# Kernel optimization log

Measured on AMD Instinct MI355X. Metric: run time of the kernel, lower is better.

Reference implementation:

```python
import jax, jax.numpy as jnp
import numpy as np

NEG = -1e20  # finite stand-in for -inf (exp underflows to 0; avoids nan grads)
S_RANGE = 19   # prune_range hard-coded in the module
TERM = 0       # termination/blank symbol
LM_ONLY = 0.25 # lm_only_scale; am_only_scale = 0 so that branch vanishes


def _mi(px, py):
    """RNN-T mutual-information forward DP (fast_rnnt mutual_information_recursion).
    px: (B,S,T+1) logprob of emitting symbol s+1 at (s,t); py: (B,S+1,T) blank logprobs.
    p[b,s,t] = logaddexp(p[b,s-1,t]+px[b,s-1,t], p[b,s,t-1]+py[b,s,t-1]); returns p[:,S,T]."""
    B, S, T1 = px.shape
    p0 = jnp.concatenate([jnp.zeros((B, 1), px.dtype),
                          jnp.cumsum(py[:, 0, :], axis=1)], axis=1)  # row s=0: (B,T+1)
    def outer(p_prev, inp):
        px_s, py_s = inp                 # (B,T+1), (B,T)
        b = p_prev + px_s                # vertical (emit) path into next row
        def inner(c, xs):
            b_t, py_t = xs
            c = jnp.logaddexp(b_t, c + py_t)
            return c, c
        _, rest = jax.lax.scan(inner, b[:, 0], (b[:, 1:].T, py_s.T))  # rest: (T,B)
        p_row = jnp.concatenate([b[:, :1], rest.T], axis=1)
        return p_row, None
    p_last, _ = jax.lax.scan(outer, p0,
                             (jnp.moveaxis(px, 1, 0), jnp.moveaxis(py[:, 1:, :], 1, 0)))
    return p_last[:, -1]  # (B,) total log-prob at (S,T)


def _smoothed_logprobs(am, lm, symbols):
    """fast_rnnt.get_rnnt_logprobs_smoothed with lm_only_scale=0.25, am_only_scale=0."""
    B, T, C = am.shape
    S = symbols.shape[1]
    lm_max = jnp.max(lm, axis=2, keepdims=True)   # (B,S+1,1)
    am_max = jnp.max(am, axis=2, keepdims=True)   # (B,T,1)
    lm_p = jnp.exp(lm - lm_max)
    am_p = jnp.exp(am - am_max)
    # normalizers[b,s,t] = log sum_k exp(lm[b,s,k] + am[b,t,k]) via matmul trick
    normalizers = jnp.log(jnp.einsum('bsc,btc->bst', lm_p, am_p)) \
        + lm_max + jnp.swapaxes(am_max, 1, 2)     # (B,S+1,T)
    sym_b = jnp.broadcast_to(symbols[:, None, :], (B, T, S))
    px_am = jnp.swapaxes(jnp.take_along_axis(am, sym_b, axis=2), 1, 2)  # (B,S,T)
    px_lm = jnp.take_along_axis(lm[:, :S], symbols[:, :, None], axis=2)  # (B,S,1)
    px = px_am + px_lm - normalizers[:, :S, :]
    lm_lsm = jax.nn.log_softmax(lm, axis=2)
    px_lmonly = jnp.take_along_axis(lm_lsm[:, :S], symbols[:, :, None], axis=2)
    comb = 1.0 - LM_ONLY
    px_i = comb * px + LM_ONLY * px_lmonly
    px_i = jnp.concatenate([px_i, jnp.full((B, S, 1), NEG, px_i.dtype)], axis=2)  # (B,S,T+1)
    py = am[:, :, TERM][:, None, :] + lm[:, :, TERM][:, :, None] - normalizers
    py_i = comb * py + LM_ONLY * lm_lsm[:, :, TERM][:, :, None]  # (B,S+1,T)
    return px_i, py_i


def _suffix_min(x):  # fast_rnnt _monotonic_lower_bound: x[t] = min(x[t:])
    return jax.lax.associative_scan(jnp.minimum, x, axis=1, reverse=True)


def _adjust_lower_bound(s_begin, r):  # fast_rnnt _adjust_pruning_lower_bound
    Tn = s_begin.shape[1]
    s_begin = _suffix_min(s_begin)
    off = (r - 1) * jnp.arange(Tn, dtype=s_begin.dtype)
    y = -(s_begin - off)
    y = jnp.maximum(_suffix_min(y), 0)
    return -(y - off)


def _prune_ranges(px_grad, py_grad, r):
    """fast_rnnt.get_rnnt_prune_ranges (all sequences full length)."""
    B, S, T1 = px_grad.shape
    T = T1 - 1
    py_pad = jnp.concatenate([py_grad, jnp.zeros((B, S + 1, 1), py_grad.dtype)], axis=2)
    tot = jnp.concatenate([px_grad, jnp.zeros((B, 1, T1), px_grad.dtype)], axis=1) + py_pad
    tot = jnp.concatenate([jnp.zeros((B, 1, T1), tot.dtype), tot], axis=1)  # (B,S+2,T1)
    cs = jnp.cumsum(tot, axis=1)
    diff = cs[:, r:, :] - cs[:, :-r, :]  # windowed occupancy sums
    s_begin = jnp.argmax(diff, axis=1)[:, :T].astype(jnp.int32)
    s_begin = _adjust_lower_bound(s_begin, r)
    return s_begin[:, :, None] + jnp.arange(r, dtype=jnp.int32)[None, None, :]  # (B,T,r)


def _pruned_logprobs(logits, symbols, ranges):
    """fast_rnnt.get_rnnt_logprobs_pruned."""
    B, T, r, C = logits.shape
    S = symbols.shape[1]
    norm = jax.nn.logsumexp(logits, axis=3)  # (B,T,r)
    sym_t = jnp.concatenate([symbols, jnp.full((B, 1), TERM, symbols.dtype)], axis=1)
    sym_b = jnp.broadcast_to(sym_t[:, None, :], (B, T, S + 1))
    pruned_sym = jnp.take_along_axis(sym_b, ranges, axis=2)  # (B,T,r)
    px = jnp.take_along_axis(logits, pruned_sym[..., None], axis=3)[..., 0] - norm
    py = logits[..., TERM] - norm
    def to_full(x):  # scatter (B,T,r) band into absolute symbol positions (B,T,S+1)
        pad = jnp.full((B, T, S + 1 - r), NEG, x.dtype)
        xf = jnp.concatenate([x, pad], axis=2)
        idx = (jnp.arange(S + 1)[None, None, :] - ranges[:, :, 0:1]) % (S + 1)
        return jnp.take_along_axis(xf, idx, axis=2)
    px_f = jnp.swapaxes(to_full(px), 1, 2)  # (B,S+1,T)
    py_f = jnp.swapaxes(to_full(py), 1, 2)  # (B,S+1,T)
    px_f = jnp.concatenate([px_f, jnp.full((B, S + 1, 1), NEG, px_f.dtype)], axis=2)[:, :S, :]
    return px_f, py_f  # (B,S,T+1), (B,S+1,T)


def _forward(am, lm, targets, joiner_w, joiner_b):
    px, py = _smoothed_logprobs(am, lm, targets)
    simple_loss = -jnp.mean(_mi(px, py))  # reduction='mean'
    # occupation-probability grads (values only, used for pruning)
    gpx, gpy = jax.grad(lambda a: jnp.sum(_mi(a[0], a[1])))(
        (jax.lax.stop_gradient(px), jax.lax.stop_gradient(py)))
    ranges = _prune_ranges(gpx, gpy, S_RANGE)  # (B,T,19) int32, constant wrt grads
    lm_pruned = jax.vmap(lambda l, rg: l[rg])(lm, ranges)  # (B,T,r,C) gather
    # joiner: logits = Linear(tanh(am_pruned + lm_pruned)); am broadcast over r
    logits = jnp.einsum('btrc,cd->btrd',
                        jnp.tanh(am[:, :, None, :] + lm_pruned), joiner_w) + joiner_b
    px2, py2 = _pruned_logprobs(logits.astype(jnp.float32), targets, ranges)
    pruned_loss = -jnp.mean(_mi(px2, py2))
    return 0.1 * simple_loss + pruned_loss


def setup_inputs() -> dict:
    key = jax.random.key(0)
    k = jax.random.split(key, 5)
    B, T, S, C = 8, 512, 128, 512
    return {
        "am": jax.random.normal(k[0], (B, T, C), jnp.float32),
        "lm": jax.random.normal(k[1], (B, S + 1, C), jnp.float32),
        "targets": jax.random.randint(k[2], (B, S), 1, C),  # blank=0 excluded
        "y_lens": jnp.full((B,), S, jnp.int32),             # full-length boundaries
        "joiner_w": 0.05 * jax.random.normal(k[3], (C, C), jnp.float32),
        "joiner_b": jnp.zeros((C,), jnp.float32),
    }


def reference(am, lm, targets, y_lens, joiner_w, joiner_b):
    # boundary = [0, 0, y_lens(=S), T] for every sequence
    return _forward(am, lm, targets, joiner_w, joiner_b)
```

## Files before the change

### kernel.cpp

```cpp
#include <hip/hip_runtime.h>
#include <math.h>

#define NEGV -1e20f
#define DPAD 132
#define RBOFF 16
#define ROWSA 676
#define RB(p,b) ((p) + ((size_t)(b) * ROWSA + RBOFF) * DPAD)

typedef __attribute__((ext_vector_type(4))) float floatx4;
typedef __attribute__((ext_vector_type(8))) short short8;
typedef __attribute__((ext_vector_type(4))) short short4v;


__device__ __forceinline__ float lae(float a, float b){
  float mx = fmaxf(a, b);
  float mn = fminf(a, b);
  return mx + __logf(1.f + __expf(mn - mx));
}

__device__ __forceinline__ short f2bf(float x){
  union { float f; unsigned u; } v; v.f = x;
  unsigned r = v.u + 0x7fffu + ((v.u >> 16) & 1u);
  return (short)(r >> 16);
}

__device__ __forceinline__ float fast_tanh(float x){
  x = fminf(fmaxf(x, -15.f), 15.f);
  float e = __expf(2.f * x);
  return (e - 1.f) / (e + 1.f);
}

__global__ __launch_bounds__(256) void k_row_stats(
    const float* __restrict__ in, float* __restrict__ outMax, float* __restrict__ outLse)
{
  int row = blockIdx.x;
  const float* r = in + (size_t)row * 512;
  int tid = threadIdx.x;
  float v0 = r[tid], v1 = r[tid + 256];
  float m = fmaxf(v0, v1);
  #pragma unroll
  for (int off = 32; off; off >>= 1) m = fmaxf(m, __shfl_xor(m, off, 64));
  __shared__ float sm[4];
  __shared__ float sbm;
  int wv = tid >> 6;
  if ((tid & 63) == 0) sm[wv] = m;
  __syncthreads();
  if (tid == 0) sbm = fmaxf(fmaxf(sm[0], sm[1]), fmaxf(sm[2], sm[3]));
  __syncthreads();
  float mx = sbm;
  if (tid == 0) outMax[row] = mx;
  if (outLse){
    float s = __expf(v0 - mx) + __expf(v1 - mx);
    #pragma unroll
    for (int off = 32; off; off >>= 1) s += __shfl_xor(s, off, 64);
    __shared__ float sp[4];
    if ((tid & 63) == 0) sp[wv] = s;
    __syncthreads();
    if (tid == 0) outLse[row] = mx + __logf(sp[0] + sp[1] + sp[2] + sp[3]);
  }
}

__global__ __launch_bounds__(256) void k_wb(const float* __restrict__ W, short* __restrict__ Wb){
  int idx = blockIdx.x * 256 + threadIdx.x;
  int d = idx >> 9, c = idx & 511;
  Wb[idx] = f2bf(W[c * 512 + d]);
}

__global__ __launch_bounds__(256) void k_norm(
    const float* __restrict__ am, const float* __restrict__ lm,
    const float* __restrict__ lmMax, const float* __restrict__ amMax,
    float* __restrict__ normv)
{
  int b = blockIdx.z;
  int s0 = blockIdx.y * 16;
  int t0 = blockIdx.x * 128;
  __shared__ float lmS[16][68];
  __shared__ float amS[128][68];
  int tid = threadIdx.x;
  int ts = tid >> 4, tt = tid & 15;
  float acc[8];
  #pragma unroll
  for (int j = 0; j < 8; ++j) acc[j] = 0.f;

  for (int k0 = 0; k0 < 512; k0 += 64){
    {
      int e = tid * 4;
      int rr = e >> 6, cc = e & 63;
      int s = s0 + rr;
      floatx4 o = {0.f, 0.f, 0.f, 0.f};
      if (s < 129){
        float mx = lmMax[b * 129 + s];
        floatx4 v = *(const floatx4*)(lm + ((size_t)(b * 129 + s)) * 512 + k0 + cc);
        o[0] = __expf(v[0] - mx); o[1] = __expf(v[1] - mx);
        o[2] = __expf(v[2] - mx); o[3] = __expf(v[3] - mx);
      }
      *(floatx4*)&lmS[rr][cc] = o;
    }
    #pragma unroll
    for (int i = 0; i < 8; ++i){
      int e = (tid + i * 256) * 4;
      int rr = e >> 6, cc = e & 63;
      float mx = amMax[b * 512 + t0 + rr];
      floatx4 v = *(const floatx4*)(am + ((size_t)(b * 512 + t0 + rr)) * 512 + k0 + cc);
      floatx4 o;
      o[0] = __expf(v[0] - mx); o[1] = __expf(v[1] - mx);
      o[2] = __expf(v[2] - mx); o[3] = __expf(v[3] - mx);
      *(floatx4*)&amS[rr][cc] = o;
    }
    __syncthreads();
    #pragma unroll 4
    for (int k = 0; k < 64; ++k){
      float a = lmS[ts][k];
      #pragma unroll
      for (int j = 0; j < 8; ++j) acc[j] += a * amS[tt + 16 * j][k];
    }
    __syncthreads();
  }
  int s = s0 + ts;
  if (s < 129){
    float lmx = lmMax[b * 129 + s];
    #pragma unroll
    for (int j = 0; j < 8; ++j){
      int t = t0 + tt + 16 * j;
      normv[((size_t)(b * 129 + s)) * 512 + t] = __logf(acc[j]) + lmx + amMax[b * 512 + t];
    }
  }
}

__global__ __launch_bounds__(256) void k_pxpy(
    const float* __restrict__ am, const float* __restrict__ lm,
    const int* __restrict__ targets, const float* __restrict__ normv,
    const float* __restrict__ lmLse, float* __restrict__ pxd, float* __restrict__ pyd)
{
  int bs = blockIdx.x;
  int b = bs / 129, s = bs % 129;
  float lm0 = lm[(size_t)bs * 512];
  float lse = lmLse[bs];
  int sym = 0; float lms = 0.f;
  if (s < 128){ sym = targets[b * 128 + s]; lms = lm[(size_t)bs * 512 + sym]; }
  const float* nrm = normv + (size_t)bs * 512;
  float* pydb = RB(pyd, b);
  float* pxdb = RB(pxd, b);
  for (int t = threadIdx.x; t < 513; t += 256){
    if (t < 512){
      float n = nrm[t];
      float a0 = am[((size_t)(b * 512 + t)) * 512];
      pydb[(size_t)(s + t) * DPAD + s] = 0.75f * (a0 + lm0 - n) + 0.25f * (lm0 - lse);
      if (s < 128){
        float as = am[((size_t)(b * 512 + t)) * 512 + sym];
        pxdb[(size_t)(s + t) * DPAD + s] = 0.75f * (as + lms - n) + 0.25f * (lms - lse);
      }
    } else if (s < 128){
      pxdb[(size_t)(s + 512) * DPAD + s] = NEGV;
    }
  }
}


__device__ __forceinline__ void dp_fwd_run(
    const float* __restrict__ pxb, const float* __restrict__ pyb,
    float* __restrict__ pab, float* __restrict__ tot, int b)
{
  int l = threadIdx.x;
  const int a = 2 * l;
  float curA = NEGV, curB = NEGV, curC = NEGV, send = NEGV;
  int paddr = (l - 1) << 2;

  float2 cpx = *(const float2*)(pxb - DPAD + a);
  float2 cpy = *(const float2*)(pyb - DPAD + a);
  float  cpz = pyb[-DPAD + 128];

  float2 b0px[8], b0py[8], b1px[8], b1py[8];
  float  b0pz[8], b1pz[8];
  float  outx[8], outy[8], outc[8];

  #pragma unroll
  for (int j = 0; j < 8; ++j){
    b0px[j] = *(const float2*)(pxb + (size_t)j * DPAD + a);
    b0py[j] = *(const float2*)(pyb + (size_t)j * DPAD + a);
    b0pz[j] = pyb[(size_t)j * DPAD + 128];
  }

  for (int i = 0; i < 40; ++i){
    int d0 = i * 16;
    #pragma unroll
    for (int j = 0; j < 8; ++j){
      b1px[j] = *(const float2*)(pxb + (size_t)(d0 + 8 + j) * DPAD + a);
      b1py[j] = *(const float2*)(pyb + (size_t)(d0 + 8 + j) * DPAD + a);
      b1pz[j] = pyb[(size_t)(d0 + 8 + j) * DPAD + 128];
    }
    #pragma unroll
    for (int j = 0; j < 8; ++j){
      int d = d0 + j;
      float2 pxm = j ? b0px[j - 1] : cpx;
      float2 pym = j ? b0py[j - 1] : cpy;
      float  pzm = j ? b0pz[j - 1] : cpz;
      float recv = __int_as_float(
          __builtin_amdgcn_ds_bpermute(paddr, __float_as_int(send)));
      int tA = d - a, tC = d - 128;
      float aaA = (l > 0) ? recv : NEGV;
      float bbA = (tA >= 1) ? curA + pym.x : NEGV;
      float nvA = lae(aaA, bbA);
      if (l == 0 && d == 0) nvA = 0.f;
      float aaB = curA + pxm.x;
      float bbB = (tA >= 2) ? curB + pym.y : NEGV;
      float nvB = lae(aaB, bbB);
      float aaC = curB + pxm.y;
      float bbC = (tC >= 1) ? curC + pzm : NEGV;
      float nvC = lae(aaC, bbC);
      if (tA >= 0 && tA <= 512) curA = nvA;
      if (tA >= 1 && tA <= 513) curB = nvB;
      if (tC >= 0 && tC <= 512) curC = nvC;
      send = curB + b0px[j].y;
      outx[j] = curA; outy[j] = curB; outc[j] = curC;
    }
    cpx = b0px[7]; cpy = b0py[7]; cpz = b0pz[7];
    if (pab){
      #pragma unroll
      for (int j = 0; j < 8; ++j)
        *(float2*)(pab + (size_t)(d0 + j) * DPAD + a) = make_float2(outx[j], outy[j]);
      if (l == 63){
        #pragma unroll
        for (int j = 0; j < 8; ++j)
          pab[(size_t)(d0 + j) * DPAD + 128] = outc[j];
      }
    }
    #pragma unroll
    for (int j = 0; j < 8; ++j){
      b0px[j] = *(const float2*)(pxb + (size_t)(d0 + 16 + j) * DPAD + a);
      b0py[j] = *(const float2*)(pyb + (size_t)(d0 + 16 + j) * DPAD + a);
      b0pz[j] = pyb[(size_t)(d0 + 16 + j) * DPAD + 128];
    }
    #pragma unroll
    for (int j = 0; j < 8; ++j){
      int d = d0 + 8 + j;
      float2 pxm = j ? b1px[j - 1] : cpx;
      float2 pym = j ? b1py[j - 1] : cpy;
      float  pzm = j ? b1pz[j - 1] : cpz;
      float recv = __int_as_float(
          __builtin_amdgcn_ds_bpermute(paddr, __float_as_int(send)));
      int tA = d - a, tC = d - 128;
      float aaA = (l > 0) ? recv : NEGV;
      float bbA = (tA >= 1) ? curA + pym.x : NEGV;
      float nvA = lae(aaA, bbA);
      float aaB = curA + pxm.x;
      float bbB = (tA >= 2) ? curB + pym.y : NEGV;
      float nvB = lae(aaB, bbB);
      float aaC = curB + pxm.y;
      float bbC = (tC >= 1) ? curC + pzm : NEGV;
      float nvC = lae(aaC, bbC);
      if (tA >= 0 && tA <= 512) curA = nvA;
      if (tA >= 1 && tA <= 513) curB = nvB;
      if (tC >= 0 && tC <= 512) curC = nvC;
      send = curB + b1px[j].y;
      outx[j] = curA; outy[j] = curB; outc[j] = curC;
    }
    cpx = b1px[7]; cpy = b1py[7]; cpz = b1pz[7];
    if (pab){
      #pragma unroll
      for (int j = 0; j < 8; ++j)
        *(float2*)(pab + (size_t)(d0 + 8 + j) * DPAD + a) = make_float2(outx[j], outy[j]);
      if (l == 63){
        #pragma unroll
        for (int j = 0; j < 8; ++j)
          pab[(size_t)(d0 + 8 + j) * DPAD + 128] = outc[j];
      }
    }
  }
  {
    float aaC = curB + cpx.y;
    float bbC = curC + cpz;
    curC = lae(aaC, bbC);
    if (l == 63){
      if (pab) pab[(size_t)640 * DPAD + 128] = curC;
      tot[b] = curC;
    }
  }
}

__device__ __forceinline__ void dp_bwd_run(
    const float* __restrict__ pxb, const float* __restrict__ pyb,
    float* __restrict__ beb)
{
  int l = threadIdx.x;
  const int a = 2 * l;
  float curA = NEGV, curB = NEGV, curC = NEGV, send = NEGV;
  int paddr = (l + 1) << 2;

  float2 b0px[8], b0py[8], b1px[8], b1py[8];
  float  b0pz[8], b1pz[8];
  float  outx[8], outy[8], outc[8];

  #pragma unroll
  for (int j = 0; j < 8; ++j){
    b0px[j] = *(const float2*)(pxb + (size_t)(640 - j) * DPAD + a);
    b0py[j] = *(const float2*)(pyb + (size_t)(640 - j) * DPAD + a);
    b0pz[j] = pyb[(size_t)(640 - j) * DPAD + 128];
  }

  for (int i = 0; i < 40; ++i){
    int d0 = 640 - 16 * i;
    #pragma unroll
    for (int j = 0; j < 8; ++j){
      b1px[j] = *(const float2*)(pxb + (size_t)(d0 - 8 - j) * DPAD + a);
      b1py[j] = *(const float2*)(pyb + (size_t)(d0 - 8 - j) * DPAD + a);
      b1pz[j] = pyb[(size_t)(d0 - 8 - j) * DPAD + 128];
    }
    #pragma unroll
    for (int j = 0; j < 8; ++j){
      int d = d0 - j;
      float2 pxA = b0px[j]; float2 pyA = b0py[j]; float pzA = b0pz[j];
      float recv = __int_as_float(
          __builtin_amdgcn_ds_bpermute(paddr, __float_as_int(send)));
      int tA = d - a, tB = tA - 1, tC = d - 128;
      float aaA = pxA.x + curB;
      float bbA = (tA <= 511) ? pyA.x + curA : NEGV;
      float nvA = lae(aaA, bbA);
      float up = (l < 63) ? recv : curC;
      float aaB = pxA.y + up;
      float bbB = (tB <= 511) ? pyA.y + curB : NEGV;
      float nvB = lae(aaB, bbB);
      float nvC = (tC <= 511) ? pzA + curC : NEGV;
      if (tC == 512) nvC = 0.f;
      if (tA >= 0 && tA <= 512) curA = nvA;
      if (tB >= 0 && tB <= 512) curB = nvB;
      if (tC >= 0 && tC <= 512) curC = nvC;
      send = curA;
      outx[j] = curA; outy[j] = curB; outc[j] = curC;
    }
    #pragma unroll
    for (int j = 0; j < 8; ++j)
      *(float2*)(beb + (size_t)(d0 - j) * DPAD + a) = make_float2(outx[j], outy[j]);
    if (l == 63){
      #pragma unroll
      for (int j = 0; j < 8; ++j)
        beb[(size_t)(d0 - j) * DPAD + 128] = outc[j];
    }
    #pragma unroll
    for (int j = 0; j < 8; ++j){
      b0px[j] = *(const float2*)(pxb + (size_t)(d0 - 16 - j) * DPAD + a);
      b0py[j] = *(const float2*)(pyb + (size_t)(d0 - 16 - j) * DPAD + a);
      b0pz[j] = pyb[(size_t)(d0 - 16 - j) * DPAD + 128];
    }
    #pragma unroll
    for (int j = 0; j < 8; ++j){
      int d = d0 - 8 - j;
      float2 pxA = b1px[j]; float2 pyA = b1py[j]; float pzA = b1pz[j];
      float recv = __int_as_float(
          __builtin_amdgcn_ds_bpermute(paddr, __float_as_int(send)));
      int tA = d - a, tB = tA - 1, tC = d - 128;
      float aaA = pxA.x + curB;
      float bbA = (tA <= 511) ? pyA.x + curA : NEGV;
      float nvA = lae(aaA, bbA);
      float up = (l < 63) ? recv : curC;
      float aaB = pxA.y + up;
      float bbB = (tB <= 511) ? pyA.y + curB : NEGV;
      float nvB = lae(aaB, bbB);
      float nvC = (tC <= 511) ? pzA + curC : NEGV;
      if (tC == 512) nvC = 0.f;
      if (tA >= 0 && tA <= 512) curA = nvA;
      if (tB >= 0 && tB <= 512) curB = nvB;
      if (tC >= 0 && tC <= 512) curC = nvC;
      send = curA;
      outx[j] = curA; outy[j] = curB; outc[j] = curC;
    }
    #pragma unroll
    for (int j = 0; j < 8; ++j)
      *(float2*)(beb + (size_t)(d0 - 8 - j) * DPAD + a) = make_float2(outx[j], outy[j]);
    if (l == 63){
      #pragma unroll
      for (int j = 0; j < 8; ++j)
        beb[(size_t)(d0 - 8 - j) * DPAD + 128] = outc[j];
    }
  }
  {
    float2 pxA = b0px[0]; float2 pyA = b0py[0]; float pzA = b0pz[0];
    float recv = __int_as_float(
        __builtin_amdgcn_ds_bpermute(paddr, __float_as_int(send)));
    int tA = -a, tB = tA - 1;
    float aaA = pxA.x + curB;
    float bbA = (tA <= 511) ? pyA.x + curA : NEGV;
    float nvA = lae(aaA, bbA);
    float up = (l < 63) ? recv : curC;
    float aaB = pxA.y + up;
    float bbB = (tB <= 511) ? pyA.y + curB : NEGV;
    float nvB = lae(aaB, bbB);
    (void)pzA;
    if (tA >= 0 && tA <= 512) curA = nvA;
    if (tB >= 0 && tB <= 512) curB = nvB;
    *(float2*)(beb + a) = make_float2(curA, curB);
    if (l == 63) beb[128] = curC;
  }
}

__global__ __launch_bounds__(64) void k_dp_fb(
    const float* __restrict__ pxd, const float* __restrict__ pyd,
    float* __restrict__ pad, float* __restrict__ betad, float* __restrict__ tots)
{
  int blk = blockIdx.x;
  if (blk < 8){
    int b = blk;
    dp_fwd_run(RB(pxd, b), RB(pyd, b), RB(pad, b), tots, b);
  } else {
    int b = blk - 8;
    dp_bwd_run(RB(pxd, b), RB(pyd, b), RB(betad, b));
  }
}

__global__ __launch_bounds__(64) void k_dp_f2(
    const float* __restrict__ pxd, const float* __restrict__ pyd,
    float* __restrict__ totp)
{
  int b = blockIdx.x;
  dp_fwd_run(RB(pxd, b), RB(pyd, b), (float*)nullptr, totp, b);
}

__global__ __launch_bounds__(256) void k_window(
    const float* __restrict__ pxd, const float* __restrict__ pyd,
    const float* __restrict__ pad, const float* __restrict__ betad,
    const float* __restrict__ tots, int* __restrict__ sbr)
{
  __shared__ float tote[129][66];
  int b = blockIdx.x >> 3;
  int t0 = (blockIdx.x & 7) << 6;
  const float* px = RB(pxd, b);
  const float* py = RB(pyd, b);
  const float* pa = RB(pad, b);
  const float* be = RB(betad, b);
  float tv = tots[b];
  int tid = threadIdx.x;
  int wv = tid >> 6, ln = tid & 63;
  for (int dd = wv; dd < 192; dd += 4){
    int d = t0 + dd;
    int slo = dd - 63 > 0 ? dd - 63 : 0;
    int shi = dd < 128 ? dd : 128;
    int s = slo + ln;
    if (s <= shi){
      size_t r0 = (size_t)d * DPAD + s, r1 = (size_t)(d + 1) * DPAD + s;
      float pav = pa[r0];
      float v = __expf(pav + py[r0] + be[r1] - tv);
      if (s < 128) v += __expf(pav + px[r0] + be[r1 + 1] - tv);
      tote[s][dd - s] = v;
    }
  }
  __syncthreads();
  if (tid < 64){
    int c = tid;
    float win = 0.f;
    for (int s = 0; s < 19; ++s) win += tote[s][c];
    float best = win; int arg = 0;
    for (int w2 = 1; w2 <= 110; ++w2){
      win += tote[w2 + 18][c] - tote[w2 - 1][c];
      if (win > best){ best = win; arg = w2; }
    }
    sbr[b * 512 + t0 + c] = arg;
  }
}

__global__ void k_adjust(const int* __restrict__ sbr, int* __restrict__ sbeg){
  if (threadIdx.x != 0) return;
  int b = blockIdx.x;
  const int* in = sbr + b * 512;
  int* out = sbeg + b * 512;
  int sbm = 1 << 30, ym = 1 << 30;
  for (int t = 511; t >= 0; --t){
    sbm = min(sbm, in[t]);
    int y = 18 * t - sbm;
    ym = min(ym, y);
    int yc = ym > 0 ? ym : 0;
    out[t] = 18 * t - yc;
  }
}

#define JROWS 64
#define HSTR  520

__global__ __launch_bounds__(256) void k_joiner(
    const float* __restrict__ am, const float* __restrict__ lm,
    const int* __restrict__ targets, const float* __restrict__ bias,
    const short* __restrict__ Wb, const int* __restrict__ sbeg,
    float* __restrict__ pxv, float* __restrict__ pyv)
{
  __shared__ short Hs[JROWS][HSTR];
  __shared__ int rowSym[JROWS];
  __shared__ int rowAm[JROWS];
  __shared__ int rowLm[JROWS];
  __shared__ float redM[JROWS][4];
  __shared__ float redS[JROWS][4];
  __shared__ float rowMax[JROWS];
  __shared__ float rowNorm[JROWS];

  int tid = threadIdx.x;
  int r0 = blockIdx.x * JROWS;
  if (tid < JROWS){
    int row = r0 + tid;
    int g = row / 19;
    int j = row - g * 19;
    int b = g >> 9;
    int t = g & 511;
    int start = sbeg[b * 512 + t];
    int sidx = start + j;
    rowSym[tid] = (sidx < 128) ? targets[b * 128 + sidx] : 0;
    rowAm[tid] = (b * 512 + t) * 512;
    rowLm[tid] = (b * 129 + sidx) * 512;
  }
  __syncthreads();

  {
    int row = tid >> 2;
    int kb = (tid & 3) * 8;
    const float* ap = am + (size_t)rowAm[row];
    const float* lp = lm + (size_t)rowLm[row];
    #pragma unroll 4
    for (int i = 0; i < 16; ++i){
      int k = kb + i * 32;
      floatx4 a0 = *(const floatx4*)(ap + k);
      floatx4 a1 = *(const floatx4*)(ap + k + 4);
      floatx4 l0 = *(const floatx4*)(lp + k);
      floatx4 l1 = *(const floatx4*)(lp + k + 4);
      short8 h;
      h[0] = f2bf(fast_tanh(a0[0] + l0[0]));
      h[1] = f2bf(fast_tanh(a0[1] + l0[1]));
      h[2] = f2bf(fast_tanh(a0[2] + l0[2]));
      h[3] = f2bf(fast_tanh(a0[3] + l0[3]));
      h[4] = f2bf(fast_tanh(a1[0] + l1[0]));
      h[5] = f2bf(fast_tanh(a1[1] + l1[1]));
      h[6] = f2bf(fast_tanh(a1[2] + l1[2]));
      h[7] = f2bf(fast_tanh(a1[3] + l1[3]));
      *(short8*)&Hs[row][k] = h;
    }
  }
  __syncthreads();

  int wv = tid >> 6, lane = tid & 63, q = lane >> 4, ln = lane & 15;
  int colBase = wv * 128 + ln;

  floatx4 acc[4][8];
  #pragma unroll
  for (int mt = 0; mt < 4; ++mt)
    #pragma unroll
    for (int nt = 0; nt < 8; ++nt) acc[mt][nt] = (floatx4){0.f, 0.f, 0.f, 0.f};

  #pragma unroll 2
  for (int k0 = 0; k0 < 512; k0 += 32){
    short8 af[4];
    #pragma unroll
    for (int mt = 0; mt < 4; ++mt)
      af[mt] = *(const short8*)&Hs[mt * 16 + ln][k0 + q * 8];
    #pragma unroll
    for (int nt = 0; nt < 8; ++nt){
      int col = colBase + nt * 16;
      short8 bfr = *(const short8*)(Wb + (size_t)col * 512 + k0 + q * 8);
      #pragma unroll
      for (int mt = 0; mt < 4; ++mt)
        acc[mt][nt] = __builtin_amdgcn_mfma_f32_16x16x32_bf16(af[mt], bfr, acc[mt][nt], 0, 0, 0);
    }
  }

  #pragma unroll
  for (int nt = 0; nt < 8; ++nt){
    float bc = bias[colBase + nt * 16];
    #pragma unroll
    for (int mt = 0; mt < 4; ++mt)
      #pragma unroll
      for (int r = 0; r < 4; ++r) acc[mt][nt][r] += bc;
  }
  #pragma unroll
  for (int mt = 0; mt < 4; ++mt)
    #pragma unroll
    for (int r = 0; r < 4; ++r){
      int row = mt * 16 + q * 4 + r;
      float m = acc[mt][0][r];
      #pragma unroll
      for (int nt = 1; nt < 8; ++nt) m = fmaxf(m, acc[mt][nt][r]);
      m = fmaxf(m, __shfl_xor(m, 1, 16));
      m = fmaxf(m, __shfl_xor(m, 2, 16));
      m = fmaxf(m, __shfl_xor(m, 4, 16));
      m = fmaxf(m, __shfl_xor(m, 8, 16));
      if (ln == 0) redM[row][wv] = m;
    }
  __syncthreads();
  if (tid < JROWS) rowMax[tid] = fmaxf(fmaxf(redM[tid][0], redM[tid][1]),
                                       fmaxf(redM[tid][2], redM[tid][3]));
  __syncthreads();
  #pragma unroll
  for (int mt = 0; mt < 4; ++mt)
    #pragma unroll
    for (int r = 0; r < 4; ++r){
      int row = mt * 16 + q * 4 + r;
      float rm = rowMax[row];
      float sa = 0.f;
      #pragma unroll
      for (int nt = 0; nt < 8; ++nt) sa += __expf(acc[mt][nt][r] - rm);
      sa += __shfl_xor(sa, 1, 16);
      sa += __shfl_xor(sa, 2, 16);
      sa += __shfl_xor(sa, 4, 16);
      sa += __shfl_xor(sa, 8, 16);
      if (ln == 0) redS[row][wv] = sa;
    }
  __syncthreads();
  if (tid < JROWS) rowNorm[tid] = rowMax[tid] +
      __logf(redS[tid][0] + redS[tid][1] + redS[tid][2] + redS[tid][3]);
  __syncthreads();
  #pragma unroll
  for (int mt = 0; mt < 4; ++mt)
    #pragma unroll
    for (int nt = 0; nt < 8; ++nt){
      int col = colBase + nt * 16;
      #pragma unroll
      for (int r = 0; r < 4; ++r){
        int row = mt * 16 + q * 4 + r;
        float v = acc[mt][nt][r] - rowNorm[row];
        int gr = r0 + row;
        if (col == 0) pyv[gr] = v;
        if (col == rowSym[row]) pxv[gr] = v;
      }
    }
}

__global__ __launch_bounds__(192) void k_band(
    const float* __restrict__ pxv, const float* __restrict__ pyv,
    const int* __restrict__ sbeg, float* __restrict__ px2d, float* __restrict__ py2d)
{
  int bd = blockIdx.x;
  int b = bd / 640, d = bd - b * 640;
  int s = threadIdx.x;
  int t = d - s;
  if (s > 128 || t < 0 || t > 512) return;
  size_t addr = ((size_t)b * ROWSA + RBOFF + d) * DPAD + s;
  if (s < 128){
    float v;
    if (t == 512) v = NEGV;
    else {
      int start = sbeg[b * 512 + t];
      int j = s - start;
      v = (j >= 0 && j < 19) ? pxv[((size_t)(b * 512 + t)) * 19 + j] : NEGV;
    }
    px2d[addr] = v;
  }
  if (t <= 511){
    int start = sbeg[b * 512 + t];
    int j = s - start;
    py2d[addr] = (j >= 0 && j < 19) ? pyv[((size_t)(b * 512 + t)) * 19 + j] : NEGV;
  }
}

__global__ void k_final(const float* __restrict__ tots, const float* __restrict__ totp,
                        float* __restrict__ out){
  if (blockIdx.x == 0 && threadIdx.x == 0){
    float a = 0.f, c = 0.f;
    for (int i = 0; i < 8; ++i){ a += tots[i]; c += totp[i]; }
    out[0] = -0.1f * (a * 0.125f) - (c * 0.125f);
  }
}

extern "C" void kernel_launch(void* const* d_in, const int* in_sizes, int n_in,
                              void* d_out, int out_size, void* d_ws, size_t ws_size,
                              hipStream_t stream){
  (void)in_sizes; (void)n_in; (void)out_size; (void)ws_size;
  const float* am      = (const float*)d_in[0];
  const float* lm      = (const float*)d_in[1];
  const int*   targets = (const int*)d_in[2];
  const float* W       = (const float*)d_in[4];
  const float* bias    = (const float*)d_in[5];
  float* out = (float*)d_out;

  char* base = (char*)d_ws;
  size_t off = 0;
  auto alloc = [&](size_t bytes) -> char* {
    char* r = base + off;
    off += (bytes + 255) & ~(size_t)255;
    return r;
  };
  const size_t DARR = 8ull * ROWSA * DPAD * 4;
  float* amMax = (float*)alloc(8ull * 512 * 4);
  float* lmMax = (float*)alloc(8ull * 129 * 4);
  float* lmLse = (float*)alloc(8ull * 129 * 4);
  float* normv = (float*)alloc(8ull * 129 * 512 * 4);
  float* pxd   = (float*)alloc(DARR);
  float* pyd   = (float*)alloc(DARR);
  float* pad   = (float*)alloc(DARR);
  float* betad = (float*)alloc(DARR);
  float* tots  = (float*)alloc(8 * 4);
  float* totp  = (float*)alloc(8 * 4);
  int*   sbr   = (int*)alloc(8ull * 512 * 4);
  int*   sbeg  = (int*)alloc(8ull * 512 * 4);
  float* pxv   = (float*)alloc(8ull * 512 * 19 * 4);
  float* pyv   = (float*)alloc(8ull * 512 * 19 * 4);
  short* Wb    = (short*)alloc(512ull * 512 * 2);
  float* px2d  = pxd;
  float* py2d  = pyd;

  k_row_stats<<<dim3(4096), dim3(256), 0, stream>>>(am, amMax, (float*)nullptr);
  k_row_stats<<<dim3(1032), dim3(256), 0, stream>>>(lm, lmMax, lmLse);
  k_wb<<<dim3(1024), dim3(256), 0, stream>>>(W, Wb);
  k_norm<<<dim3(4, 9, 8), dim3(256), 0, stream>>>(am, lm, lmMax, amMax, normv);
  k_pxpy<<<dim3(1032), dim3(256), 0, stream>>>(am, lm, targets, normv, lmLse, pxd, pyd);
  k_dp_fb<<<dim3(16), dim3(64), 0, stream>>>(pxd, pyd, pad, betad, tots);
  k_window<<<dim3(64), dim3(256), 0, stream>>>(pxd, pyd, pad, betad, tots, sbr);
  k_adjust<<<dim3(8), dim3(64), 0, stream>>>(sbr, sbeg);
  k_joiner<<<dim3(1216), dim3(256), 0, stream>>>(am, lm, targets, bias, Wb, sbeg, pxv, pyv);
  k_band<<<dim3(5120), dim3(192), 0, stream>>>(pxv, pyv, sbeg, px2d, py2d);
  k_dp_f2<<<dim3(8), dim3(64), 0, stream>>>(px2d, py2d, totp);
  k_final<<<dim3(1), dim3(64), 0, stream>>>(tots, totp, out);
}
```

Baseline: 632.9 us.

## Split joiner into H staging, 2D-tiled GEMM with partial softmax, and finalize

The fused joiner kernel, which built tanh activations in LDS and ran a 64x512 tile per block, is split into three kernels. The first writes bf16 tanh activations to global memory. The second runs a 128x128 output-tiled MFMA GEMM over a 2D grid and emits per-column-block partial max/sum-exp plus raw px/py logits. The third merges the partials into the log-softmax normalizer. The aim is smaller per-block register tiles, more blocks in flight and better reuse of W tiles, at the cost of an extra HBM round trip for H (about 80 MB) and two extra launches. The tanh helper also drops its clamp and uses a reciprocal form.

```diff
diff --git a/kernel.cpp b/kernel.cpp
--- a/kernel.cpp
+++ b/kernel.cpp
@@ -6,10 +6,10 @@
 #define RBOFF 16
 #define ROWSA 676
 #define RB(p,b) ((p) + ((size_t)(b) * ROWSA + RBOFF) * DPAD)
+#define NROWS 77824
 
 typedef __attribute__((ext_vector_type(4))) float floatx4;
 typedef __attribute__((ext_vector_type(8))) short short8;
-typedef __attribute__((ext_vector_type(4))) short short4v;
 
 
 __device__ __forceinline__ float lae(float a, float b){
@@ -24,10 +24,9 @@
   return (short)(r >> 16);
 }
 
-__device__ __forceinline__ float fast_tanh(float x){
-  x = fminf(fmaxf(x, -15.f), 15.f);
+__device__ __forceinline__ float tanh5(float x){
   float e = __expf(2.f * x);
-  return (e - 1.f) / (e + 1.f);
+  return 1.f - 2.f * __builtin_amdgcn_rcpf(e + 1.f);
 }
 
 __global__ __launch_bounds__(256) void k_row_stats(
@@ -374,7 +373,7 @@
     }
   }
   {
-    float2 pxA = b0px[0]; float2 pyA = b0py[0]; float pzA = b0pz[0];
+    float2 pxA = b0px[0]; float2 pyA = b0py[0];
     float recv = __int_as_float(
         __builtin_amdgcn_ds_bpermute(paddr, __float_as_int(send)));
     int tA = -a, tB = tA - 1;
@@ -385,7 +384,6 @@
     float aaB = pxA.y + up;
     float bbB = (tB <= 511) ? pyA.y + curB : NEGV;
     float nvB = lae(aaB, bbB);
-    (void)pzA;
     if (tA >= 0 && tA <= 512) curA = nvA;
     if (tB >= 0 && tB <= 512) curB = nvB;
     *(float2*)(beb + a) = make_float2(curA, curB);
@@ -472,150 +470,168 @@
   }
 }
 
-#define JROWS 64
-#define HSTR  520
-
-__global__ __launch_bounds__(256) void k_joiner(
+__global__ __launch_bounds__(256) void k_stageH(
     const float* __restrict__ am, const float* __restrict__ lm,
-    const int* __restrict__ targets, const float* __restrict__ bias,
-    const short* __restrict__ Wb, const int* __restrict__ sbeg,
-    float* __restrict__ pxv, float* __restrict__ pyv)
-{
-  __shared__ short Hs[JROWS][HSTR];
-  __shared__ int rowSym[JROWS];
-  __shared__ int rowAm[JROWS];
-  __shared__ int rowLm[JROWS];
-  __shared__ float redM[JROWS][4];
-  __shared__ float redS[JROWS][4];
-  __shared__ float rowMax[JROWS];
-  __shared__ float rowNorm[JROWS];
-
+    const int* __restrict__ sbeg, short* __restrict__ Hb)
+{
+  __shared__ int rowAm[64], rowLm[64];
   int tid = threadIdx.x;
-  int r0 = blockIdx.x * JROWS;
-  if (tid < JROWS){
+  int r0 = blockIdx.x * 64;
+  if (tid < 64){
     int row = r0 + tid;
     int g = row / 19;
     int j = row - g * 19;
-    int b = g >> 9;
-    int t = g & 511;
-    int start = sbeg[b * 512 + t];
-    int sidx = start + j;
-    rowSym[tid] = (sidx < 128) ? targets[b * 128 + sidx] : 0;
+    int b = g >> 9, t = g & 511;
+    int sidx = sbeg[b * 512 + t] + j;
     rowAm[tid] = (b * 512 + t) * 512;
     rowLm[tid] = (b * 129 + sidx) * 512;
   }
   __syncthreads();
-
-  {
-    int row = tid >> 2;
-    int kb = (tid & 3) * 8;
-    const float* ap = am + (size_t)rowAm[row];
-    const float* lp = lm + (size_t)rowLm[row];
-    #pragma unroll 4
-    for (int i = 0; i < 16; ++i){
-      int k = kb + i * 32;
-      floatx4 a0 = *(const floatx4*)(ap + k);
-      floatx4 a1 = *(const floatx4*)(ap + k + 4);
-      floatx4 l0 = *(const floatx4*)(lp + k);
-      floatx4 l1 = *(const floatx4*)(lp + k + 4);
-      short8 h;
-      h[0] = f2bf(fast_tanh(a0[0] + l0[0]));
-      h[1] = f2bf(fast_tanh(a0[1] + l0[1]));
-      h[2] = f2bf(fast_tanh(a0[2] + l0[2]));
-      h[3] = f2bf(fast_tanh(a0[3] + l0[3]));
-      h[4] = f2bf(fast_tanh(a1[0] + l1[0]));
-      h[5] = f2bf(fast_tanh(a1[1] + l1[1]));
-      h[6] = f2bf(fast_tanh(a1[2] + l1[2]));
-      h[7] = f2bf(fast_tanh(a1[3] + l1[3]));
-      *(short8*)&Hs[row][k] = h;
-    }
+  int row = tid >> 2;
+  int kb = (tid & 3) * 8;
+  const float* ap = am + (size_t)rowAm[row];
+  const float* lp = lm + (size_t)rowLm[row];
+  short* hp = Hb + (size_t)(r0 + row) * 512;
+  #pragma unroll 4
+  for (int i = 0; i < 16; ++i){
+    int k = kb + i * 32;
+    floatx4 a0 = *(const floatx4*)(ap + k);
+    floatx4 a1 = *(const floatx4*)(ap + k + 4);
+    floatx4 l0 = *(const floatx4*)(lp + k);
+    floatx4 l1 = *(const floatx4*)(lp + k + 4);
+    short8 h;
+    h[0] = f2bf(tanh5(a0[0] + l0[0]));
+    h[1] = f2bf(tanh5(a0[1] + l0[1]));
+    h[2] = f2bf(tanh5(a0[2] + l0[2]));
+    h[3] = f2bf(tanh5(a0[3] + l0[3]));
+    h[4] = f2bf(tanh5(a1[0] + l1[0]));
+    h[5] = f2bf(tanh5(a1[1] + l1[1]));
+    h[6] = f2bf(tanh5(a1[2] + l1[2]));
+    h[7] = f2bf(tanh5(a1[3] + l1[3]));
+    *(short8*)(hp + k) = h;
+  }
+}
+
+__global__ __launch_bounds__(256) void k_jgemm(
+    const short* __restrict__ Hb, const short* __restrict__ Wb,
+    const float* __restrict__ bias, const int* __restrict__ targets,
+    const int* __restrict__ sbeg,
+    float2* __restrict__ pms, float* __restrict__ pxraw, float* __restrict__ pyraw)
+{
+  __shared__ int rowSym[128];
+  __shared__ float redM[128][2];
+  __shared__ float redS[128][2];
+  __shared__ float rowM[128];
+
+  int tid = threadIdx.x;
+  int rt = blockIdx.x;
+  int nb = blockIdx.y;
+  int r0 = rt * 128, c0 = nb * 128;
+  if (tid < 128){
+    int row = r0 + tid;
+    int g = row / 19;
+    int j = row - g * 19;
+    int b = g >> 9, t = g & 511;
+    int sidx = sbeg[b * 512 + t] + j;
+    rowSym[tid] = (sidx < 128) ? targets[b * 128 + sidx] : 0;
   }
   __syncthreads();
 
-  int wv = tid >> 6, lane = tid & 63, q = lane >> 4, ln = lane & 15;
-  int colBase = wv * 128 + ln;
-
-  floatx4 acc[4][8];
+  int w = tid >> 6, lane = tid & 63, q = lane >> 4, ln = lane & 15;
+  int mBase = (w & 1) * 64;
+  int nBase = (w >> 1) * 64;
+  const short* Ab = Hb + (size_t)(r0 + mBase + ln) * 512 + q * 8;
+  const short* Bb = Wb + (size_t)(c0 + nBase + ln) * 512 + q * 8;
+
+  floatx4 acc[4][4];
   #pragma unroll
   for (int mt = 0; mt < 4; ++mt)
     #pragma unroll
-    for (int nt = 0; nt < 8; ++nt) acc[mt][nt] = (floatx4){0.f, 0.f, 0.f, 0.f};
+    for (int nt = 0; nt < 4; ++nt) acc[mt][nt] = (floatx4){0.f, 0.f, 0.f, 0.f};
 
   #pragma unroll 2
   for (int k0 = 0; k0 < 512; k0 += 32){
-    short8 af[4];
+    short8 af[4], bf[4];
     #pragma unroll
     for (int mt = 0; mt < 4; ++mt)
-      af[mt] = *(const short8*)&Hs[mt * 16 + ln][k0 + q * 8];
-    #pragma unroll
-    for (int nt = 0; nt < 8; ++nt){
-      int col = colBase + nt * 16;
-      short8 bfr = *(const short8*)(Wb + (size_t)col * 512 + k0 + q * 8);
+      af[mt] = *(const short8*)(Ab + (size_t)mt * 16 * 512 + k0);
+    #pragma unroll
+    for (int nt = 0; nt < 4; ++nt)
+      bf[nt] = *(const short8*)(Bb + (size_t)nt * 16 * 512 + k0);
+    #pragma unroll
+    for (int nt = 0; nt < 4; ++nt)
       #pragma unroll
       for (int mt = 0; mt < 4; ++mt)
-        acc[mt][nt] = __builtin_amdgcn_mfma_f32_16x16x32_bf16(af[mt], bfr, acc[mt][nt], 0, 0, 0);
-    }
+        acc[mt][nt] = __builtin_amdgcn_mfma_f32_16x16x32_bf16(af[mt], bf[nt], acc[mt][nt], 0, 0, 0);
   }
 
   #pragma unroll
-  for (int nt = 0; nt < 8; ++nt){
-    float bc = bias[colBase + nt * 16];
+  for (int nt = 0; nt < 4; ++nt){
+    int col = c0 + nBase + nt * 16 + ln;
+    float bc = bias[col];
     #pragma unroll
     for (int mt = 0; mt < 4; ++mt)
       #pragma unroll
-      for (int r = 0; r < 4; ++r) acc[mt][nt][r] += bc;
+      for (int r = 0; r < 4; ++r){
+        float v = acc[mt][nt][r] + bc;
+        acc[mt][nt][r] = v;
+        int rl = mBase + mt * 16 + q * 4 + r;
+        if (col == 0) pyraw[r0 + rl] = v;
+        if (col == rowSym[rl]) pxraw[r0 + rl] = v;
+      }
   }
   #pragma unroll
   for (int mt = 0; mt < 4; ++mt)
     #pragma unroll
     for (int r = 0; r < 4; ++r){
-      int row = mt * 16 + q * 4 + r;
+      int rl = mBase + mt * 16 + q * 4 + r;
       float m = acc[mt][0][r];
       #pragma unroll
-      for (int nt = 1; nt < 8; ++nt) m = fmaxf(m, acc[mt][nt][r]);
+      for (int nt = 1; nt < 4; ++nt) m = fmaxf(m, acc[mt][nt][r]);
       m = fmaxf(m, __shfl_xor(m, 1, 16));
       m = fmaxf(m, __shfl_xor(m, 2, 16));
       m = fmaxf(m, __shfl_xor(m, 4, 16));
       m = fmaxf(m, __shfl_xor(m, 8, 16));
-      if (ln == 0) redM[row][wv] = m;
+      if (ln == 0) redM[rl][w >> 1] = m;
     }
   __syncthreads();
-  if (tid < JROWS) rowMax[tid] = fmaxf(fmaxf(redM[tid][0], redM[tid][1]),
-                                       fmaxf(redM[tid][2], redM[tid][3]));
+  if (tid < 128) rowM[tid] = fmaxf(redM[tid][0], redM[tid][1]);
   __syncthreads();
   #pragma unroll
   for (int mt = 0; mt < 4; ++mt)
     #pragma unroll
     for (int r = 0; r < 4; ++r){
-      int row = mt * 16 + q * 4 + r;
-      float rm = rowMax[row];
+      int rl = mBase + mt * 16 + q * 4 + r;
+      float rm = rowM[rl];
       float sa = 0.f;
       #pragma unroll
-      for (int nt = 0; nt < 8; ++nt) sa += __expf(acc[mt][nt][r] - rm);
+      for (int nt = 0; nt < 4; ++nt) sa += __expf(acc[mt][nt][r] - rm);
       sa += __shfl_xor(sa, 1, 16);
       sa += __shfl_xor(sa, 2, 16);
       sa += __shfl_xor(sa, 4, 16);
       sa += __shfl_xor(sa, 8, 16);
-      if (ln == 0) redS[row][wv] = sa;
+      if (ln == 0) redS[rl][w >> 1] = sa;
     }
   __syncthreads();
-  if (tid < JROWS) rowNorm[tid] = rowMax[tid] +
-      __logf(redS[tid][0] + redS[tid][1] + redS[tid][2] + redS[tid][3]);
-  __syncthreads();
-  #pragma unroll
-  for (int mt = 0; mt < 4; ++mt)
-    #pragma unroll
-    for (int nt = 0; nt < 8; ++nt){
-      int col = colBase + nt * 16;
-      #pragma unroll
-      for (int r = 0; r < 4; ++r){
-        int row = mt * 16 + q * 4 + r;
-        float v = acc[mt][nt][r] - rowNorm[row];
-        int gr = r0 + row;
-        if (col == 0) pyv[gr] = v;
-        if (col == rowSym[row]) pxv[gr] = v;
-      }
-    }
+  if (tid < 128)
+    pms[(size_t)nb * NROWS + r0 + tid] = make_float2(rowM[tid], redS[tid][0] + redS[tid][1]);
+}
+
+__global__ __launch_bounds__(256) void k_jfin(
+    const float2* __restrict__ pms, const float* __restrict__ pxraw,
+    const float* __restrict__ pyraw, float* __restrict__ pxv, float* __restrict__ pyv)
+{
+  int row = blockIdx.x * 256 + threadIdx.x;
+  float2 p0 = pms[row];
+  float2 p1 = pms[NROWS + row];
+  float2 p2 = pms[2 * NROWS + row];
+  float2 p3 = pms[3 * NROWS + row];
+  float M = fmaxf(fmaxf(p0.x, p1.x), fmaxf(p2.x, p3.x));
+  float S = p0.y * __expf(p0.x - M) + p1.y * __expf(p1.x - M)
+          + p2.y * __expf(p2.x - M) + p3.y * __expf(p3.x - M);
+  float norm = M + __logf(S);
+  pxv[row] = pxraw[row] - norm;
+  pyv[row] = pyraw[row] - norm;
 }
 
 __global__ __launch_bounds__(192) void k_band(
@@ -685,9 +701,13 @@
   float* totp  = (float*)alloc(8 * 4);
   int*   sbr   = (int*)alloc(8ull * 512 * 4);
   int*   sbeg  = (int*)alloc(8ull * 512 * 4);
-  float* pxv   = (float*)alloc(8ull * 512 * 19 * 4);
-  float* pyv   = (float*)alloc(8ull * 512 * 19 * 4);
+  float* pxv   = (float*)alloc((size_t)NROWS * 4);
+  float* pyv   = (float*)alloc((size_t)NROWS * 4);
   short* Wb    = (short*)alloc(512ull * 512 * 2);
+  short* Hb    = (short*)alloc((size_t)NROWS * 512 * 2);
+  float2* pms  = (float2*)alloc(4ull * NROWS * 8);
+  float* pxraw = (float*)alloc((size_t)NROWS * 4);
+  float* pyraw = (float*)alloc((size_t)NROWS * 4);
   float* px2d  = pxd;
   float* py2d  = pyd;
 
@@ -699,7 +719,9 @@
   k_dp_fb<<<dim3(16), dim3(64), 0, stream>>>(pxd, pyd, pad, betad, tots);
   k_window<<<dim3(64), dim3(256), 0, stream>>>(pxd, pyd, pad, betad, tots, sbr);
   k_adjust<<<dim3(8), dim3(64), 0, stream>>>(sbr, sbeg);
-  k_joiner<<<dim3(1216), dim3(256), 0, stream>>>(am, lm, targets, bias, Wb, sbeg, pxv, pyv);
+  k_stageH<<<dim3(1216), dim3(256), 0, stream>>>(am, lm, sbeg, Hb);
+  k_jgemm<<<dim3(608, 4), dim3(256), 0, stream>>>(Hb, Wb, bias, targets, sbeg, pms, pxraw, pyraw);
+  k_jfin<<<dim3(304), dim3(256), 0, stream>>>(pms, pxraw, pyraw, pxv, pyv);
   k_band<<<dim3(5120), dim3(192), 0, stream>>>(pxv, pyv, sbeg, px2d, py2d);
   k_dp_f2<<<dim3(8), dim3(64), 0, stream>>>(px2d, py2d, totp);
   k_final<<<dim3(1), dim3(64), 0, stream>>>(tots, totp, out);
```

Result: slower. 646.8 us (+2.2%).
